# Performance work log

Hardware: AMD Instinct MI355X
Metric: run time of the kernel (lower is better)

The kernel has to match this reference:

```python
import jax, jax.numpy as jnp
import numpy as np

B, N, E, Q = 4, 10000, 160000, 256
D, M, U, H, P = 128, 64, 126, 128, 7  # node_dim, msg_sz, update_sz, mlp hidden, pose dim
MSG_STEPS = 3
NUM_COPIES = 1


def setup_inputs() -> dict:
    key = jax.random.key(0)
    ks = jax.random.split(key, 12)
    return {
        "nodes_states": jax.random.normal(ks[0], (B, N, D), jnp.float32),
        "query_poses": jax.random.normal(ks[1], (B, Q, P), jnp.float32),
        "attn": jax.random.uniform(ks[2], (B, Q, N), jnp.float32) / N,
        "edge_sources": jax.random.randint(ks[3], (E,), 0, N),
        "edge_sinks": jax.random.randint(ks[4], (E,), 0, N),
        "w1e": jax.random.normal(ks[5], (2 * D, H), jnp.float32) * 0.05,
        "b1e": jnp.zeros((H,), jnp.float32),
        "w2e": jax.random.normal(ks[6], (H, M), jnp.float32) * 0.05,
        "b2e": jnp.zeros((M,), jnp.float32),
        "w1n": jax.random.normal(ks[7], (D + M, H), jnp.float32) * 0.05,
        "b1n": jnp.zeros((H,), jnp.float32),
        "w2n": jax.random.normal(ks[8], (H, U), jnp.float32) * 0.05,
        "b2n": jnp.zeros((U,), jnp.float32),
    }


def reference(nodes_states, query_poses, attn, edge_sources, edge_sinks,
              w1e, b1e, w2e, b2e, w1n, b1n, w2n, b2n):
    def step(states, _):
        # gather endpoint states: [B, E, 2*D]
        einp = jnp.concatenate([states[:, edge_sources], states[:, edge_sinks]], axis=-1)
        # edge MLP -> per-edge messages [B, E, M]
        msg = jax.nn.relu(einp @ w1e + b1e) @ w2e + b2e
        # scatter-add messages to sink nodes [B, N, M]
        incoming = jnp.zeros((states.shape[0], N, M), states.dtype).at[:, edge_sinks].add(msg)
        # node MLP update [B, N, U]
        ninp = jnp.concatenate([incoming, states], axis=-1)
        upd = jax.nn.relu(ninp @ w1n + b1n) @ w2n + b2n
        # only the last U channels (state part, not positions) are updated
        states = states.at[:, :, -U:].add(upd)
        return states, None

    states, _ = jax.lax.scan(step, nodes_states, None, length=MSG_STEPS)
    extraction = jnp.einsum('bqn,bnd->bqd', attn, states)  # interpolation readout
    return jnp.concatenate([query_poses] * NUM_COPIES + [extraction], axis=-1)
```

## Files before the change

### kernel.cpp

```cpp
#include <hip/hip_runtime.h>

#define Bx 4
#define Nn 10000
#define Ee 160000
#define Qq 256
#define Dd 128
#define Mm 64
#define Uu 126
#define Hh 128
#define Pp 7

#define KG 1252

typedef unsigned short u16;
typedef __bf16 bf16x8 __attribute__((ext_vector_type(8)));
typedef float f32x4 __attribute__((ext_vector_type(4)));

__device__ __forceinline__ float b2f(u16 h){
  unsigned u = ((unsigned)h) << 16; float f; __builtin_memcpy(&f, &u, 4); return f;
}
__device__ __forceinline__ u16 f2b(float f){
  __bf16 h = (__bf16)f; u16 r; __builtin_memcpy(&r, &h, 2); return r;
}
__device__ __forceinline__ float ldin(const void* p, long i, int flag){
  return flag ? b2f(((const u16*)p)[i]) : ((const float*)p)[i];
}

__global__ void probe_kernel(const void* in0, int* flag){
  if (threadIdx.x == 0 && blockIdx.x == 0){
    const u16* p = (const u16*)in0;
    int cnt = 0;
    for (int i = 0; i < 256; i++){
      float a = fabsf(b2f(p[i]));
      if (a > 0.0009765625f && a < 32.0f) cnt++;
    }
    *flag = (cnt >= 240) ? 1 : 0;
  }
}

__global__ void prep_kernel(const void* w1e, const void* b1e, const void* w2e, const void* b2e,
                            const void* w1n, const void* b1n, const void* w2n, const void* b2n,
                            const int* __restrict__ flag,
                            u16* w1e_s, u16* w2e_s, u16* w1n_s, u16* w2n_s,
                            float* b1e_f, float* b2e_f, float* b1n_f, float* b2n_f)
{
  int f = *flag;
  for (int idx = blockIdx.x * blockDim.x + threadIdx.x; idx < 82368; idx += gridDim.x * blockDim.x){
    if (idx < 32768){
      int k = idx >> 7, h = idx & 127;
      w1e_s[(k >> 3) * 1024 + h * 8 + (k & 7)] = f2b(ldin(w1e, idx, f));
    } else if (idx < 40960){
      int i2 = idx - 32768; int k = i2 >> 6, m2 = i2 & 63;
      w2e_s[(k >> 3) * 512 + m2 * 8 + (k & 7)] = f2b(ldin(w2e, i2, f));
    } else if (idx < 65536){
      int i2 = idx - 40960; int k = i2 >> 7, h = i2 & 127;
      w1n_s[(k >> 3) * 1024 + h * 8 + (k & 7)] = f2b(ldin(w1n, i2, f));
    } else if (idx < 81920){
      int i2 = idx - 65536; int k = i2 >> 7, u = i2 & 127;
      float v = (u < 126) ? ldin(w2n, (long)k * 126 + u, f) : 0.f;
      w2n_s[(k >> 3) * 1024 + u * 8 + (k & 7)] = f2b(v);
    } else if (idx < 82048){ b1e_f[idx - 81920] = ldin(b1e, idx - 81920, f); }
    else if (idx < 82112){ b2e_f[idx - 82048] = ldin(b2e, idx - 82048, f); }
    else if (idx < 82240){ b1n_f[idx - 82112] = ldin(b1n, idx - 82112, f); }
    else { int j = idx - 82240; b2n_f[j] = (j < 126) ? ldin(b2n, j, f) : 0.f; }
  }
}

__global__ void init_states_kernel(const void* in0, const int* __restrict__ flag,
                                   const int* __restrict__ snk,
                                   float* __restrict__ sf, u16* __restrict__ sbm,
                                   int* __restrict__ cnt)
{
  int f = *flag;
  const long total = (long)Bx * Nn * Dd;
  long base = (long)blockIdx.x * blockDim.x + threadIdx.x;
  for (long i = base; i < total; i += (long)gridDim.x * blockDim.x){
    float v = ldin(in0, i, f);
    sf[i] = v; sbm[i] = f2b(v);
  }
  for (long i = base; i < Ee; i += (long)gridDim.x * blockDim.x)
    atomicAdd(&cnt[snk[(int)i]], 1);
}

__global__ void scan_kernel(const int* __restrict__ cnt, int* __restrict__ rowp){
  __shared__ int tot[1024];
  int t = threadIdx.x;
  int base = t * 10;
  int local[10]; int s = 0;
  #pragma unroll
  for (int i = 0; i < 10; i++){
    int v = (base + i < Nn) ? cnt[base + i] : 0;
    local[i] = s; s += v;
  }
  tot[t] = s;
  __syncthreads();
  for (int o = 1; o < 1024; o <<= 1){
    int v = (t >= o) ? tot[t - o] : 0;
    __syncthreads();
    tot[t] += v;
    __syncthreads();
  }
  int prefix = (t == 0) ? 0 : tot[t - 1];
  #pragma unroll
  for (int i = 0; i < 10; i++)
    if (base + i < Nn) rowp[base + i] = prefix + local[i];
  if (t == 1023) rowp[Nn] = tot[1023];
}
__global__ void fill_kernel(const int* __restrict__ src, const int* __restrict__ snk,
                            const int* __restrict__ rowp, int* __restrict__ cnt,
                            int* __restrict__ psrc){
  int i = blockIdx.x * blockDim.x + threadIdx.x;
  if (i < Ee){
    int s = snk[i];
    int p = rowp[s] + atomicAdd(&cnt[s], 1);
    psrc[p] = src[i];
  }
}

__global__ __launch_bounds__(256) void xform_kernel(
  const u16* __restrict__ sbm, const u16* __restrict__ w1s,
  const float* __restrict__ b1f, u16* __restrict__ xab)
{
  __shared__ __align__(16) u16 w1h[16384];
  __shared__ __align__(16) u16 Yt[64 * 136];
  int tid = threadIdx.x;
  int b = (blockIdx.x & 7) >> 1;
  int nt = ((blockIdx.x >> 3) << 1) + (blockIdx.x & 1);
  if (nt >= 157) return;
  int n0 = nt * 64;
  int w = tid >> 6, lane = tid & 63, m = lane & 15, quad = lane >> 4;
  int n = n0 + w * 16 + m;
  int nld = n < Nn ? n : Nn - 1;
  const u16* srow = sbm + (((size_t)b * Nn + nld) << 7);

  bf16x8 a[4];
  #pragma unroll
  for (int lk = 0; lk < 4; lk++) a[lk] = *(const bf16x8*)(srow + lk * 32 + quad * 8);

  const f32x4 z4 = {0.f, 0.f, 0.f, 0.f};
  int row_l = lane >> 2, seg = lane & 3;
  int nst = n0 + w * 16 + row_l;

  #pragma unroll
  for (int half = 0; half < 2; half++){
    __syncthreads();
    {
      const uint4* g = (const uint4*)(w1s + half * 16384);
      uint4* l = (uint4*)w1h;
      #pragma unroll
      for (int i = 0; i < 8; i++) l[tid + i * 256] = g[tid + i * 256];
    }
    __syncthreads();
    f32x4 acc[8];
    #pragma unroll
    for (int ct = 0; ct < 8; ct++) acc[ct] = z4;
    #pragma unroll
    for (int lk = 0; lk < 4; lk++){
      #pragma unroll
      for (int ct = 0; ct < 8; ct++){
        bf16x8 bv = *(const bf16x8*)(w1h + (((lk * 4 + quad) << 7) + ct * 16 + m) * 8);
        acc[ct] = __builtin_amdgcn_mfma_f32_16x16x32_bf16(a[lk], bv, acc[ct], 0, 0, 0);
      }
    }
    #pragma unroll
    for (int ct = 0; ct < 8; ct++){
      float bb = (half == 0) ? b1f[ct * 16 + m] : 0.f;
      #pragma unroll
      for (int i = 0; i < 4; i++)
        Yt[(w * 16 + quad * 4 + i) * 136 + ct * 16 + m] = f2b(acc[ct][i] + bb);
    }
    if (nst < Nn){
      const u16* tb = Yt + (w * 16 + row_l) * 136 + seg * 8;
      uint4 x0 = *(const uint4*)(tb);
      uint4 x1 = *(const uint4*)(tb + 32);
      uint4 x2 = *(const uint4*)(tb + 64);
      uint4 x3 = *(const uint4*)(tb + 96);
      u16* gb = xab + ((size_t)b * Nn + nst) * 256 + half * 128 + seg * 8;
      *(uint4*)(gb)      = x0;
      *(uint4*)(gb + 32) = x1;
      *(uint4*)(gb + 64) = x2;
      *(uint4*)(gb + 96) = x3;
    }
  }
}

__global__ __launch_bounds__(256) void node_kernel(
  float* __restrict__ sf, u16* __restrict__ sbm, const u16* __restrict__ xab,
  const int* __restrict__ rowp, const int* __restrict__ psrc,
  const u16* __restrict__ w2es, const float* __restrict__ b2ef,
  const u16* __restrict__ w1s, const u16* __restrict__ w2s,
  const float* __restrict__ b1f, const float* __restrict__ b2f2)
{
  __shared__ __align__(16) u16 ninp[64 * 200];
  __shared__ __align__(16) u16 hsYt[64 * 136];
  int b = (blockIdx.x & 7) >> 1;
  int nt = ((blockIdx.x >> 3) << 1) + (blockIdx.x & 1);
  if (nt >= 157) return;
  int n0 = nt * 64;
  int tid = threadIdx.x;

  {
    int nl = tid >> 2, part = tid & 3;
    int n = n0 + nl;
    float acc[32];
    #pragma unroll
    for (int i = 0; i < 32; i++) acc[i] = 0.f;
    if (n < Nn){
      float xbf[32];
      {
        const u16* xp = xab + ((size_t)b * Nn + n) * 256 + 128 + part * 8;
        union { uint4 v; u16 h[8]; } q[4];
        q[0].v = *(const uint4*)(xp);
        q[1].v = *(const uint4*)(xp + 32);
        q[2].v = *(const uint4*)(xp + 64);
        q[3].v = *(const uint4*)(xp + 96);
        #pragma unroll
        for (int t4 = 0; t4 < 4; t4++)
          #pragma unroll
          for (int j = 0; j < 8; j++) xbf[t4 * 8 + j] = b2f(q[t4].h[j]);
      }
      int r0 = rowp[n], r1 = rowp[n + 1];
      const u16* xb0 = xab + (size_t)b * Nn * 256 + part * 8;
      for (int r = r0; r < r1; r++){
        int s = psrc[r];
        const u16* xs = xb0 + (size_t)s * 256;
        union { uint4 v; u16 h[8]; } q[4];
        q[0].v = *(const uint4*)(xs);
        q[1].v = *(const uint4*)(xs + 32);
        q[2].v = *(const uint4*)(xs + 64);
        q[3].v = *(const uint4*)(xs + 96);
        #pragma unroll
        for (int t4 = 0; t4 < 4; t4++)
          #pragma unroll
          for (int j = 0; j < 8; j++){
            float v = b2f(q[t4].h[j]) + xbf[t4 * 8 + j];
            acc[t4 * 8 + j] += v > 0.f ? v : 0.f;
          }
      }
    }
    union { u16 h[32]; uint4 v[4]; } hb;
    #pragma unroll
    for (int i = 0; i < 32; i++) hb.h[i] = f2b(acc[i]);
    u16* hp = hsYt + nl * 136 + part * 8;
    *(uint4*)(hp)      = hb.v[0];
    *(uint4*)(hp + 32) = hb.v[1];
    *(uint4*)(hp + 64) = hb.v[2];
    *(uint4*)(hp + 96) = hb.v[3];
    u16* dp = ninp + nl * 200 + 64 + part * 8;
    if (n < Nn){
      const u16* sp = sbm + (((size_t)b * Nn + n) << 7) + part * 8;
      *(uint4*)(dp)      = *(const uint4*)(sp);
      *(uint4*)(dp + 32) = *(const uint4*)(sp + 32);
      *(uint4*)(dp + 64) = *(const uint4*)(sp + 64);
      *(uint4*)(dp + 96) = *(const uint4*)(sp + 96);
    } else {
      uint4 zz = {0, 0, 0, 0};
      *(uint4*)(dp)      = zz;
      *(uint4*)(dp + 32) = zz;
      *(uint4*)(dp + 64) = zz;
      *(uint4*)(dp + 96) = zz;
    }
  }

  int w = tid >> 6, lane = tid & 63, m = lane & 15, quad = lane >> 4;
  const f32x4 z4 = {0.f, 0.f, 0.f, 0.f};

  {
    f32x4 acc[4];
    #pragma unroll
    for (int ct = 0; ct < 4; ct++) acc[ct] = z4;
    #pragma unroll
    for (int ks = 0; ks < 4; ks++){
      bf16x8 a = *(const bf16x8*)(hsYt + (w * 16 + m) * 136 + ks * 32 + quad * 8);
      #pragma unroll
      for (int ct = 0; ct < 4; ct++){
        bf16x8 bv = *(const bf16x8*)(w2es + (((ks * 4 + quad) << 6) + ct * 16 + m) * 8);
        acc[ct] = __builtin_amdgcn_mfma_f32_16x16x32_bf16(a, bv, acc[ct], 0, 0, 0);
      }
    }
    #pragma unroll
    for (int i = 0; i < 4; i++){
      int n = n0 + w * 16 + quad * 4 + i;
      float deg = (n < Nn) ? (float)(rowp[n + 1] - rowp[n]) : 0.f;
      #pragma unroll
      for (int ct = 0; ct < 4; ct++)
        ninp[(w * 16 + quad * 4 + i) * 200 + ct * 16 + m] = f2b(acc[ct][i] + deg * b2ef[ct * 16 + m]);
    }
  }

  f32x4 acc1[8];
  #pragma unroll
  for (int ct = 0; ct < 8; ct++) acc1[ct] = z4;
  #pragma unroll 1
  for (int ks = 0; ks < 6; ks++){
    bf16x8 a = *(const bf16x8*)(ninp + (w * 16 + m) * 200 + ks * 32 + quad * 8);
    #pragma unroll
    for (int ct = 0; ct < 8; ct++){
      bf16x8 bv = *(const bf16x8*)(w1s + (((ks * 4 + quad) << 7) + ct * 16 + m) * 8);
      acc1[ct] = __builtin_amdgcn_mfma_f32_16x16x32_bf16(a, bv, acc1[ct], 0, 0, 0);
    }
  }
  #pragma unroll
  for (int ct = 0; ct < 8; ct++){
    float bb = b1f[ct * 16 + m];
    #pragma unroll
    for (int i = 0; i < 4; i++){
      float v = acc1[ct][i] + bb;
      v = v > 0.f ? v : 0.f;
      hsYt[(w * 16 + quad * 4 + i) * 136 + ct * 16 + m] = f2b(v);
    }
  }
  f32x4 acc2[8];
  #pragma unroll
  for (int ct = 0; ct < 8; ct++) acc2[ct] = z4;
  #pragma unroll 1
  for (int ko = 0; ko < 4; ko++){
    bf16x8 a2 = *(const bf16x8*)(hsYt + (w * 16 + m) * 136 + ko * 32 + quad * 8);
    #pragma unroll
    for (int ct = 0; ct < 8; ct++){
      bf16x8 bv = *(const bf16x8*)(w2s + (((ko * 4 + quad) << 7) + ct * 16 + m) * 8);
      acc2[ct] = __builtin_amdgcn_mfma_f32_16x16x32_bf16(a2, bv, acc2[ct], 0, 0, 0);
    }
  }
  #pragma unroll
  for (int ct = 0; ct < 8; ct++){
    int u = ct * 16 + m;
    if (u < 126){
      float bb = b2f2[u];
      #pragma unroll
      for (int i = 0; i < 4; i++){
        int n = n0 + w * 16 + quad * 4 + i;
        if (n < Nn){
          size_t idx = (((size_t)b * Nn + n) << 7) + 2 + u;
          float v = sf[idx] + acc2[ct][i] + bb;
          sf[idx] = v;
          sbm[idx] = f2b(v);
        }
      }
    }
  }
}

__global__ void swz_s_kernel(const u16* __restrict__ sbm, u16* __restrict__ sswz)
{
  const long total = (long)Bx * KG * 128;
  for (long i = (long)blockIdx.x * blockDim.x + threadIdx.x; i < total; i += (long)gridDim.x * blockDim.x){
    int d = (int)(i & 127); long r = i >> 7;
    int kg = (int)(r % KG); int b = (int)(r / KG);
    union { u16 h[8]; uint4 v[2]; } t;
    if (kg < 1250){
      #pragma unroll
      for (int j = 0; j < 8; j++)
        t.h[j] = sbm[(((size_t)b * Nn + kg * 8 + j) << 7) + d];
    } else {
      #pragma unroll
      for (int j = 0; j < 8; j++) t.h[j] = 0;
    }
    *(uint4*)(sswz + i * 8) = t.v[0];
    *(uint4*)(sswz + i * 8 + 8) = t.v[1];
  }
}
__global__ __launch_bounds__(256) void extract2_kernel(
  const void* __restrict__ attn, const int* __restrict__ flag,
  const u16* __restrict__ sswz, float* __restrict__ part)
{
  int f = *flag;
  int blk = blockIdx.x;
  int kc = blk & 31, qt = (blk >> 5) & 3, b = blk >> 7;
  int tid = threadIdx.x, w = tid >> 6, lane = tid & 63, m = lane & 15, quad = lane >> 4;
  int qr = qt * 4 + w, q0 = qr * 16;
  int kg0 = kc * 40;
  int nsteps = (kc == 31) ? 3 : 10;
  long arow = ((long)(b * Qq + q0 + m)) * Nn;
  const u16* ab16 = (const u16*)attn + arow;
  const float* af32 = (const float*)attn + arow;
  const u16* sbase = sswz + ((size_t)b) * KG * 1024;
  f32x4 acc[8];
  const f32x4 z4 = {0.f, 0.f, 0.f, 0.f};
  #pragma unroll
  for (int ct = 0; ct < 8; ct++) acc[ct] = z4;
  #pragma unroll 1
  for (int t = 0; t < nsteps; t++){
    int kg = kg0 + t * 4 + quad;
    int kgc = kg < KG ? kg : 0;
    bf16x8 a;
    if (kg < 1250){
      if (f){
        a = *(const bf16x8*)(ab16 + kg * 8);
      } else {
        const float* ap = af32 + kg * 8;
        float4 p0 = *(const float4*)ap;
        float4 p1 = *(const float4*)(ap + 4);
        a[0] = (__bf16)p0.x; a[1] = (__bf16)p0.y; a[2] = (__bf16)p0.z; a[3] = (__bf16)p0.w;
        a[4] = (__bf16)p1.x; a[5] = (__bf16)p1.y; a[6] = (__bf16)p1.z; a[7] = (__bf16)p1.w;
      }
    } else {
      #pragma unroll
      for (int j = 0; j < 8; j++) a[j] = (__bf16)0.f;
    }
    #pragma unroll
    for (int ct = 0; ct < 8; ct++){
      bf16x8 bv = *(const bf16x8*)(sbase + ((size_t)kgc * 128 + ct * 16 + m) * 8);
      acc[ct] = __builtin_amdgcn_mfma_f32_16x16x32_bf16(a, bv, acc[ct], 0, 0, 0);
    }
  }
  #pragma unroll
  for (int ct = 0; ct < 8; ct++){
    #pragma unroll
    for (int i = 0; i < 4; i++)
      part[(((size_t)(kc * 4 + b)) * Qq + q0 + quad * 4 + i) * 128 + ct * 16 + m] = acc[ct][i];
  }
}

__global__ void final_kernel(const void* __restrict__ poses, const int* __restrict__ flag,
                             const float* __restrict__ part, void* __restrict__ out)
{
  int f = *flag;
  const long total = (long)Bx * Qq * (Pp + Dd);
  for (long idx = (long)blockIdx.x * blockDim.x + threadIdx.x; idx < total; idx += (long)gridDim.x * blockDim.x){
    int j = (int)(idx % (Pp + Dd));
    long bq = idx / (Pp + Dd);
    float v;
    if (j < Pp){
      v = ldin(poses, bq * Pp + j, f);
    } else {
      int dd = j - Pp;
      int b = (int)(bq >> 8), q = (int)(bq & 255);
      v = 0.f;
      #pragma unroll
      for (int kc = 0; kc < 32; kc++)
        v += part[(((size_t)(kc * 4 + b) * Qq + q) << 7) + dd];
    }
    if (f) ((u16*)out)[idx] = f2b(v);
    else ((float*)out)[idx] = v;
  }
}

extern "C" void kernel_launch(void* const* d_in, const int* in_sizes, int n_in,
                              void* d_out, int out_size, void* d_ws, size_t ws_size,
                              hipStream_t stream)
{
  const void* in_states = d_in[0];
  const void* in_poses  = d_in[1];
  const void* in_attn   = d_in[2];
  const int*  in_src    = (const int*)d_in[3];
  const int*  in_snk    = (const int*)d_in[4];
  const void* in_w1e = d_in[5];  const void* in_b1e = d_in[6];
  const void* in_w2e = d_in[7];  const void* in_b2e = d_in[8];
  const void* in_w1n = d_in[9];  const void* in_b1n = d_in[10];
  const void* in_w2n = d_in[11]; const void* in_b2n = d_in[12];

  char* ws = (char*)d_ws;
  size_t off = 0;
  auto alloc = [&](size_t bytes){ size_t o = off; off = (off + bytes + 255) & ~(size_t)255; return o; };
  size_t o_sf   = alloc((size_t)Bx * Nn * Dd * 4);
  size_t o_sb   = alloc((size_t)Bx * Nn * Dd * 2);
  size_t o_xab  = alloc((size_t)Bx * Nn * 256 * 2);
  size_t o_rowp = alloc((size_t)(Nn + 1) * 4);
  size_t o_rcnt = alloc((size_t)Nn * 4);
  size_t o_psrc = alloc((size_t)Ee * 4);
  size_t o_w1e  = alloc(32768 * 2);
  size_t o_w2e  = alloc(8192 * 2);
  size_t o_w1n  = alloc(24576 * 2);
  size_t o_w2n  = alloc(16384 * 2);
  size_t o_b1e  = alloc(128 * 4);
  size_t o_b2e  = alloc(64 * 4);
  size_t o_b1n  = alloc(128 * 4);
  size_t o_b2n  = alloc(128 * 4);
  size_t o_flag = alloc(4);

  size_t sswzB = (size_t)Bx * KG * 128 * 8 * 2;
  size_t partB = (size_t)32 * Bx * Qq * Dd * 4;
  size_t o_sswz = alloc(sswzB);
  size_t o_part = alloc(partB);

  float* sf    = (float*)(ws + o_sf);
  u16*   sbm   = (u16*)(ws + o_sb);
  u16*   xab   = (u16*)(ws + o_xab);
  int*   rowp  = (int*)(ws + o_rowp);
  int*   rcnt  = (int*)(ws + o_rcnt);
  int*   psrc  = (int*)(ws + o_psrc);
  u16*   w1e_s = (u16*)(ws + o_w1e);
  u16*   w2e_s = (u16*)(ws + o_w2e);
  u16*   w1n_s = (u16*)(ws + o_w1n);
  u16*   w2n_s = (u16*)(ws + o_w2n);
  float* b1e_f = (float*)(ws + o_b1e);
  float* b2e_f = (float*)(ws + o_b2e);
  float* b1n_f = (float*)(ws + o_b1n);
  float* b2n_f = (float*)(ws + o_b2n);
  int*   flag  = (int*)(ws + o_flag);
  u16*   sswz  = (u16*)(ws + o_sswz);
  float* part  = (float*)(ws + o_part);

  hipMemsetAsync(rcnt, 0, (size_t)Nn * 4, stream);
  probe_kernel<<<1, 64, 0, stream>>>(in_states, flag);
  prep_kernel<<<322, 256, 0, stream>>>(in_w1e, in_b1e, in_w2e, in_b2e,
                                       in_w1n, in_b1n, in_w2n, in_b2n, flag,
                                       w1e_s, w2e_s, w1n_s, w2n_s,
                                       b1e_f, b2e_f, b1n_f, b2n_f);
  init_states_kernel<<<1024, 256, 0, stream>>>(in_states, flag, in_snk, sf, sbm, rcnt);

  scan_kernel<<<1, 1024, 0, stream>>>(rcnt, rowp);
  hipMemsetAsync(rcnt, 0, (size_t)Nn * 4, stream);
  fill_kernel<<<(Ee + 255) / 256, 256, 0, stream>>>(in_src, in_snk, rowp, rcnt, psrc);

  for (int step = 0; step < 3; step++){
    xform_kernel<<<632, 256, 0, stream>>>(sbm, w1e_s, b1e_f, xab);
    node_kernel<<<632, 256, 0, stream>>>(sf, sbm, xab, rowp, psrc,
                                         w2e_s, b2e_f,
                                         w1n_s, w2n_s, b1n_f, b2n_f);
  }
  swz_s_kernel<<<2504, 256, 0, stream>>>(sbm, sswz);
  extract2_kernel<<<512, 256, 0, stream>>>(in_attn, flag, sswz, part);
  final_kernel<<<540, 256, 0, stream>>>(in_poses, flag, part, d_out);
}
```

Baseline: 363.1 us.

## Sort nodes by degree and split node tiles across more threads

A one-block sort_kernel buckets nodes by in-degree in descending order and writes a permutation. node_kernel then processes nodes in that order, so nodes in a wave have similar edge-loop trip counts and less time is lost to divergence. The node tile also shrinks from 64 to 32 nodes with 8 threads per node in the gather phase, and the grid doubles. The cost is an extra indirection and scattered state writes through the permutation, and only half the threads take part in the MFMA phase.

```diff
diff --git a/kernel.cpp b/kernel.cpp
--- a/kernel.cpp
+++ b/kernel.cpp
@@ -116,6 +116,29 @@
     psrc[p] = src[i];
   }
 }
+__global__ void sort_kernel(const int* __restrict__ rowp, int* __restrict__ perm){
+  __shared__ int hist[64], off[64];
+  int t = threadIdx.x;
+  if (t < 64) hist[t] = 0;
+  __syncthreads();
+  for (int n = t; n < Nn; n += 1024){
+    int d = rowp[n + 1] - rowp[n];
+    int bin = d > 63 ? 0 : 63 - d;
+    atomicAdd(&hist[bin], 1);
+  }
+  __syncthreads();
+  if (t == 0){
+    int s = 0;
+    for (int i = 0; i < 64; i++){ off[i] = s; s += hist[i]; }
+  }
+  __syncthreads();
+  for (int n = t; n < Nn; n += 1024){
+    int d = rowp[n + 1] - rowp[n];
+    int bin = d > 63 ? 0 : 63 - d;
+    int p = atomicAdd(&off[bin], 1);
+    perm[p] = n;
+  }
+}
 
 __global__ __launch_bounds__(256) void xform_kernel(
   const u16* __restrict__ sbm, const u16* __restrict__ w1s,
@@ -187,83 +210,82 @@
 __global__ __launch_bounds__(256) void node_kernel(
   float* __restrict__ sf, u16* __restrict__ sbm, const u16* __restrict__ xab,
   const int* __restrict__ rowp, const int* __restrict__ psrc,
+  const int* __restrict__ perm,
   const u16* __restrict__ w2es, const float* __restrict__ b2ef,
   const u16* __restrict__ w1s, const u16* __restrict__ w2s,
   const float* __restrict__ b1f, const float* __restrict__ b2f2)
 {
-  __shared__ __align__(16) u16 ninp[64 * 200];
-  __shared__ __align__(16) u16 hsYt[64 * 136];
-  int b = (blockIdx.x & 7) >> 1;
-  int nt = ((blockIdx.x >> 3) << 1) + (blockIdx.x & 1);
-  if (nt >= 157) return;
-  int n0 = nt * 64;
+  __shared__ __align__(16) u16 ninp[32 * 200];
+  __shared__ __align__(16) u16 hsYt[32 * 136];
+  int b = blockIdx.x & 3;
+  int nt = blockIdx.x >> 2;
+  int n0 = nt * 32;
   int tid = threadIdx.x;
 
   {
-    int nl = tid >> 2, part = tid & 3;
+    int nl = tid >> 3, part = tid & 7;
     int n = n0 + nl;
-    float acc[32];
-    #pragma unroll
-    for (int i = 0; i < 32; i++) acc[i] = 0.f;
+    float acc[16];
+    #pragma unroll
+    for (int i = 0; i < 16; i++) acc[i] = 0.f;
+    int pn = 0;
     if (n < Nn){
-      float xbf[32];
+      pn = perm[n];
+      float xbf[16];
       {
-        const u16* xp = xab + ((size_t)b * Nn + n) * 256 + 128 + part * 8;
-        union { uint4 v; u16 h[8]; } q[4];
-        q[0].v = *(const uint4*)(xp);
-        q[1].v = *(const uint4*)(xp + 32);
-        q[2].v = *(const uint4*)(xp + 64);
-        q[3].v = *(const uint4*)(xp + 96);
+        const u16* xp = xab + ((size_t)b * Nn + pn) * 256 + 128 + part * 8;
+        union { uint4 v; u16 h[8]; } q0, q1;
+        q0.v = *(const uint4*)(xp);
+        q1.v = *(const uint4*)(xp + 64);
         #pragma unroll
-        for (int t4 = 0; t4 < 4; t4++)
-          #pragma unroll
-          for (int j = 0; j < 8; j++) xbf[t4 * 8 + j] = b2f(q[t4].h[j]);
+        for (int j = 0; j < 8; j++){ xbf[j] = b2f(q0.h[j]); xbf[8 + j] = b2f(q1.h[j]); }
       }
-      int r0 = rowp[n], r1 = rowp[n + 1];
+      int r0 = rowp[pn], r1 = rowp[pn + 1];
       const u16* xb0 = xab + (size_t)b * Nn * 256 + part * 8;
       for (int r = r0; r < r1; r++){
         int s = psrc[r];
         const u16* xs = xb0 + (size_t)s * 256;
-        union { uint4 v; u16 h[8]; } q[4];
-        q[0].v = *(const uint4*)(xs);
-        q[1].v = *(const uint4*)(xs + 32);
-        q[2].v = *(const uint4*)(xs + 64);
-        q[3].v = *(const uint4*)(xs + 96);
+        union { uint4 v; u16 h[8]; } q0, q1;
+        q0.v = *(const uint4*)(xs);
+        q1.v = *(const uint4*)(xs + 64);
         #pragma unroll
-        for (int t4 = 0; t4 < 4; t4++)
-          #pragma unroll
-          for (int j = 0; j < 8; j++){
-            float v = b2f(q[t4].h[j]) + xbf[t4 * 8 + j];
-            acc[t4 * 8 + j] += v > 0.f ? v : 0.f;
-          }
+        for (int j = 0; j < 8; j++){
+          float v0 = b2f(q0.h[j]) + xbf[j];
+          acc[j] += v0 > 0.f ? v0 : 0.f;
+          float v1 = b2f(q1.h[j]) + xbf[8 + j];
+          acc[8 + j] += v1 > 0.f ? v1 : 0.f;
+        }
       }
     }
-    union { u16 h[32]; uint4 v[4]; } hb;
-    #pragma unroll
-    for (int i = 0; i < 32; i++) hb.h[i] = f2b(acc[i]);
+    union { u16 h[16]; uint4 v[2]; } hb;
+    #pragma unroll
+    for (int i = 0; i < 16; i++) hb.h[i] = f2b(acc[i]);
     u16* hp = hsYt + nl * 136 + part * 8;
     *(uint4*)(hp)      = hb.v[0];
-    *(uint4*)(hp + 32) = hb.v[1];
-    *(uint4*)(hp + 64) = hb.v[2];
-    *(uint4*)(hp + 96) = hb.v[3];
+    *(uint4*)(hp + 64) = hb.v[1];
     u16* dp = ninp + nl * 200 + 64 + part * 8;
     if (n < Nn){
-      const u16* sp = sbm + (((size_t)b * Nn + n) << 7) + part * 8;
+      const u16* sp = sbm + (((size_t)b * Nn + pn) << 7) + part * 8;
       *(uint4*)(dp)      = *(const uint4*)(sp);
-      *(uint4*)(dp + 32) = *(const uint4*)(sp + 32);
       *(uint4*)(dp + 64) = *(const uint4*)(sp + 64);
-      *(uint4*)(dp + 96) = *(const uint4*)(sp + 96);
     } else {
       uint4 zz = {0, 0, 0, 0};
       *(uint4*)(dp)      = zz;
-      *(uint4*)(dp + 32) = zz;
       *(uint4*)(dp + 64) = zz;
-      *(uint4*)(dp + 96) = zz;
-    }
-  }
+    }
+  }
+  __syncthreads();
+  if (tid >= 128) return;
 
   int w = tid >> 6, lane = tid & 63, m = lane & 15, quad = lane >> 4;
   const f32x4 z4 = {0.f, 0.f, 0.f, 0.f};
+
+  int pnv[4];
+  #pragma unroll
+  for (int i = 0; i < 4; i++){
+    int n = n0 + w * 16 + quad * 4 + i;
+    pnv[i] = (n < Nn) ? perm[n] : -1;
+  }
 
   {
     f32x4 acc[4];
@@ -280,8 +302,7 @@
     }
     #pragma unroll
     for (int i = 0; i < 4; i++){
-      int n = n0 + w * 16 + quad * 4 + i;
-      float deg = (n < Nn) ? (float)(rowp[n + 1] - rowp[n]) : 0.f;
+      float deg = (pnv[i] >= 0) ? (float)(rowp[pnv[i] + 1] - rowp[pnv[i]]) : 0.f;
       #pragma unroll
       for (int ct = 0; ct < 4; ct++)
         ninp[(w * 16 + quad * 4 + i) * 200 + ct * 16 + m] = f2b(acc[ct][i] + deg * b2ef[ct * 16 + m]);
@@ -329,9 +350,8 @@
       float bb = b2f2[u];
       #pragma unroll
       for (int i = 0; i < 4; i++){
-        int n = n0 + w * 16 + quad * 4 + i;
-        if (n < Nn){
-          size_t idx = (((size_t)b * Nn + n) << 7) + 2 + u;
+        if (pnv[i] >= 0){
+          size_t idx = (((size_t)b * Nn + pnv[i]) << 7) + 2 + u;
           float v = sf[idx] + acc2[ct][i] + bb;
           sf[idx] = v;
           sbm[idx] = f2b(v);
@@ -459,6 +479,7 @@
   size_t o_rowp = alloc((size_t)(Nn + 1) * 4);
   size_t o_rcnt = alloc((size_t)Nn * 4);
   size_t o_psrc = alloc((size_t)Ee * 4);
+  size_t o_perm = alloc((size_t)Nn * 4);
   size_t o_w1e  = alloc(32768 * 2);
   size_t o_w2e  = alloc(8192 * 2);
   size_t o_w1n  = alloc(24576 * 2);
@@ -480,6 +501,7 @@
   int*   rowp  = (int*)(ws + o_rowp);
   int*   rcnt  = (int*)(ws + o_rcnt);
   int*   psrc  = (int*)(ws + o_psrc);
+  int*   perm  = (int*)(ws + o_perm);
   u16*   w1e_s = (u16*)(ws + o_w1e);
   u16*   w2e_s = (u16*)(ws + o_w2e);
   u16*   w1n_s = (u16*)(ws + o_w1n);
@@ -503,12 +525,13 @@
   scan_kernel<<<1, 1024, 0, stream>>>(rcnt, rowp);
   hipMemsetAsync(rcnt, 0, (size_t)Nn * 4, stream);
   fill_kernel<<<(Ee + 255) / 256, 256, 0, stream>>>(in_src, in_snk, rowp, rcnt, psrc);
+  sort_kernel<<<1, 1024, 0, stream>>>(rowp, perm);
 
   for (int step = 0; step < 3; step++){
     xform_kernel<<<632, 256, 0, stream>>>(sbm, w1e_s, b1e_f, xab);
-    node_kernel<<<632, 256, 0, stream>>>(sf, sbm, xab, rowp, psrc,
-                                         w2e_s, b2e_f,
-                                         w1n_s, w2n_s, b1n_f, b2n_f);
+    node_kernel<<<1252, 256, 0, stream>>>(sf, sbm, xab, rowp, psrc, perm,
+                                          w2e_s, b2e_f,
+                                          w1n_s, w2n_s, b1n_f, b2n_f);
   }
   swz_s_kernel<<<2504, 256, 0, stream>>>(sbm, sswz);
   extract2_kernel<<<512, 256, 0, stream>>>(in_attn, flag, sswz, part);
```

New measurement: 372.0 us. 2.5% more time.
